# Kernel optimization log

Measured on AMD Instinct MI355X. Metric: run time of the kernel, lower is better.

## Reference

```python
import jax, jax.numpy as jnp
import numpy as np

N_NODES = 100000
N_EDGES = 1600000
D_IN = 128
D_HID = 128
D_OUT = 128
ORIG = 90000


def setup_inputs() -> dict:
    key = jax.random.key(0)
    ks = jax.random.split(key, 8)
    x = jax.random.normal(ks[0], (N_NODES, D_IN), dtype=jnp.float32)
    edge_index = jax.random.randint(ks[1], (2, N_EDGES), 0, N_NODES, dtype=jnp.int64)
    # Glorot-ish scaled weights; PyG SAGEConv: lin_l (with bias) on aggregated, lin_r (no bias) on root
    s1 = 1.0 / np.sqrt(D_IN)
    s2 = 1.0 / np.sqrt(D_HID)
    Wl1 = jax.random.normal(ks[2], (D_IN, D_HID), dtype=jnp.float32) * s1
    bl1 = jnp.zeros((D_HID,), dtype=jnp.float32)
    Wr1 = jax.random.normal(ks[3], (D_IN, D_HID), dtype=jnp.float32) * s1
    Wl2 = jax.random.normal(ks[4], (D_HID, D_OUT), dtype=jnp.float32) * s2
    bl2 = jnp.zeros((D_OUT,), dtype=jnp.float32)
    Wr2 = jax.random.normal(ks[5], (D_HID, D_OUT), dtype=jnp.float32) * s2
    return {"x": x, "edge_index": edge_index, "original_size": ORIG,
            "Wl1": Wl1, "bl1": bl1, "Wr1": Wr1,
            "Wl2": Wl2, "bl2": bl2, "Wr2": Wr2}


def _sage_conv(x, src, dst, Wl, bl, Wr):
    # PyG SAGEConv (aggr='mean'): out = lin_l(mean_{j in N(i)} x_j) + lin_r(x_i)
    n = x.shape[0]
    msgs = x[src]                                            # [E, d] gather
    ssum = jax.ops.segment_sum(msgs, dst, num_segments=n)    # [N, d]
    cnt = jax.ops.segment_sum(jnp.ones((src.shape[0],), dtype=x.dtype), dst,
                              num_segments=n)                # [N]
    mean = ssum / jnp.maximum(cnt, 1.0)[:, None]             # 0 for isolated nodes
    return mean @ Wl + bl + x @ Wr


def reference(x, edge_index, original_size, Wl1, bl1, Wr1, Wl2, bl2, Wr2):
    src, dst = edge_index[0], edge_index[1]
    h = _sage_conv(x, src, dst, Wl1, bl1, Wr1)
    h = _sage_conv(h, src, dst, Wl2, bl2, Wr2)
    return h[:original_size]
```

## Files before the change

### kernel.cpp

```cpp
#include <hip/hip_runtime.h>

#define NN 100000
#define DD 128

typedef __attribute__((ext_vector_type(8))) short bf16x8;
typedef __attribute__((ext_vector_type(4))) float f32x4;

__device__ __forceinline__ float bf2f(unsigned short u) {
    union { unsigned int i; float f; } v;
    v.i = ((unsigned int)u) << 16;
    return v.f;
}

__device__ __forceinline__ unsigned short f2bf(float f) {
    union { float f; unsigned int i; } v;
    v.f = f;
    unsigned int x = v.i;
    return (unsigned short)((x + 0x7FFFu + ((x >> 16) & 1u)) >> 16);
}

__device__ __forceinline__ float2 load2(const float* p, int i2) {
    return ((const float2*)p)[i2];
}

__device__ __forceinline__ bf16x8 load8_bf(const unsigned short* p) {
    return *((const bf16x8*)p);
}
__device__ __forceinline__ bf16x8 load8_bf(const float* p) {
    float4 a = ((const float4*)p)[0];
    float4 b = ((const float4*)p)[1];
    bf16x8 r;
    r[0] = (short)f2bf(a.x); r[1] = (short)f2bf(a.y);
    r[2] = (short)f2bf(a.z); r[3] = (short)f2bf(a.w);
    r[4] = (short)f2bf(b.x); r[5] = (short)f2bf(b.y);
    r[6] = (short)f2bf(b.z); r[7] = (short)f2bf(b.w);
    return r;
}


#define PCH 16
#define NBUKMAX 512
#define CAP 12288

__global__ __launch_bounds__(256) void hist_buckets(
    const int* __restrict__ ei, int E, int* __restrict__ bcnt, int nbuk) {
    __shared__ int is64_s;
    __shared__ int hl[NBUKMAX];
    int tid = threadIdx.x;
    for (int i = tid; i < nbuk; i += 256) hl[i] = 0;
    if (tid < 64) {
        int ok = (ei[2 * tid + 1] == 0);
        int all = __all(ok);
        if (tid == 0) is64_s = all;
    }
    __syncthreads();
    int is64 = is64_s;
    int e0 = blockIdx.x * (256 * PCH) + tid;
#pragma unroll
    for (int c = 0; c < PCH; c++) {
        int e = e0 + c * 256;
        if (e < E) {
            int d = is64 ? ei[2 * (E + e)] : ei[E + e];
            atomicAdd(&hl[d >> 8], 1);
        }
    }
    __syncthreads();
    for (int i = tid; i < nbuk; i += 256) {
        int v = hl[i];
        if (v) atomicAdd(&bcnt[i], v);
    }
}

__global__ void scan_buckets(const int* __restrict__ bcnt, int nbuk,
                             int* __restrict__ boff, int* __restrict__ offN, int E) {
    __shared__ int wsum[8];
    int tid = threadIdx.x;
    int lane = tid & 63, wid = tid >> 6;
    int v = (tid < nbuk) ? bcnt[tid] : 0;
    int s = v;
#pragma unroll
    for (int dl = 1; dl < 64; dl <<= 1) {
        int t = __shfl_up(s, dl, 64);
        if (lane >= dl) s += t;
    }
    if (lane == 63) wsum[wid] = s;
    __syncthreads();
    int w = 0;
#pragma unroll
    for (int i = 0; i < 8; i++) w += (i < wid) ? wsum[i] : 0;
    if (tid < nbuk) boff[tid] = w + s - v;
    if (tid == nbuk - 1) boff[nbuk] = w + s;
    if (tid == 0) offN[0] = E;
}

__global__ __launch_bounds__(256) void partition_edges(
    const int* __restrict__ ei, int E, const int* __restrict__ boff,
    int* __restrict__ bcur, unsigned long long* __restrict__ pairs, int nbuk) {
    __shared__ int is64_s;
    __shared__ int cntb[NBUKMAX];
    __shared__ int baseb[NBUKMAX];
    __shared__ int boffb[NBUKMAX];
    int tid = threadIdx.x;
    for (int i = tid; i < nbuk; i += 256) {
        cntb[i] = 0;
        boffb[i] = boff[i];
    }
    if (tid < 64) {
        int ok = (ei[2 * tid + 1] == 0);
        int all = __all(ok);
        if (tid == 0) is64_s = all;
    }
    __syncthreads();
    int is64 = is64_s;
    int e0 = blockIdx.x * (256 * PCH) + tid;

    int dv[PCH], sv[PCH], bl[PCH];
    bool va[PCH];
#pragma unroll
    for (int c = 0; c < PCH; c++) {
        int e = e0 + c * 256;
        va[c] = (e < E);
        dv[c] = va[c] ? (is64 ? ei[2 * (E + e)] : ei[E + e]) : 0;
        sv[c] = va[c] ? (is64 ? ei[2 * e] : ei[e]) : 0;
        bl[c] = 0;
    }
#pragma unroll
    for (int c = 0; c < PCH; c++) {
        if (va[c]) {
            int b = dv[c] >> 8;
            int l = atomicAdd(&cntb[b], 1);
            bl[c] = (b << 16) | l;
        }
    }
    __syncthreads();
    for (int i = tid; i < nbuk; i += 256) {
        int cb = cntb[i];
        baseb[i] = cb ? atomicAdd(&bcur[i], cb) : 0;
    }
    __syncthreads();
#pragma unroll
    for (int c = 0; c < PCH; c++) {
        if (va[c]) {
            int b = bl[c] >> 16, l = bl[c] & 0xffff;
            pairs[(size_t)(boffb[b] + baseb[b] + l)] =
                ((unsigned long long)(unsigned int)dv[c] << 32) | (unsigned int)sv[c];
        }
    }
}

__global__ __launch_bounds__(256) void build_csr(
    const unsigned long long* __restrict__ pairs, const int* __restrict__ boff,
    int* __restrict__ off, int* __restrict__ csr, int* __restrict__ cur, int N) {
    int b = blockIdx.x;
    int lo = b << 8;
    if (lo >= N) return;
    int hi = min(lo + 256, N);
    int nn = hi - lo;
    int base = boff[b];
    int pcount = boff[b + 1] - base;

    __shared__ int cnt_l[256];
    __shared__ int start_l[256];
    __shared__ int cur_l[256];
    __shared__ int wsum[4];
    __shared__ int lds_csr[CAP];

    int tid = threadIdx.x;
    cnt_l[tid] = 0;
    __syncthreads();

    for (int i = tid; i < pcount; i += 256) {
        int d = (int)(pairs[base + i] >> 32);
        atomicAdd(&cnt_l[d - lo], 1);
    }
    __syncthreads();

    int v = cnt_l[tid];
    int s = v;
    int lane = tid & 63, wid = tid >> 6;
#pragma unroll
    for (int dl = 1; dl < 64; dl <<= 1) {
        int t = __shfl_up(s, dl, 64);
        if (lane >= dl) s += t;
    }
    if (lane == 63) wsum[wid] = s;
    __syncthreads();
    int w = 0;
#pragma unroll
    for (int i = 0; i < 4; i++) w += (i < wid) ? wsum[i] : 0;
    int excl = w + s - v;
    start_l[tid] = excl;
    cur_l[tid] = excl;
    if (tid < nn) off[lo + tid] = base + excl;
    __syncthreads();

    if (pcount <= CAP) {
        for (int i = tid; i < pcount; i += 256) {
            unsigned long long p = pairs[base + i];
            int d = (int)(p >> 32) - lo;
            int pos = atomicAdd(&cur_l[d], 1);
            lds_csr[pos] = (int)(p & 0xffffffffu);
        }
        __syncthreads();
        for (int i = tid; i < pcount; i += 256) csr[base + i] = lds_csr[i];
    } else {
        for (int i = tid; i < pcount; i += 256) {
            unsigned long long p = pairs[base + i];
            int dg = (int)(p >> 32);
            int q = atomicAdd(&cur[dg], 1);
            csr[base + start_l[dg - lo] + q] = (int)(p & 0xffffffffu);
        }
    }
}

__global__ void cast_bf16(const float* __restrict__ in, unsigned short* __restrict__ out,
                          int n4) {
    int i = blockIdx.x * blockDim.x + threadIdx.x;
    if (i >= n4) return;
    float4 v = ((const float4*)in)[i];
    ushort4 o;
    o.x = f2bf(v.x); o.y = f2bf(v.y); o.z = f2bf(v.z); o.w = f2bf(v.w);
    ((ushort4*)out)[i] = o;
}

__global__ void prep_weights(const float* __restrict__ Wl1, const float* __restrict__ Wr1,
                             const float* __restrict__ Wl2, const float* __restrict__ Wr2,
                             unsigned short* __restrict__ Wt1, unsigned short* __restrict__ Wt2) {
    __shared__ float t[32][33];
    int which = blockIdx.x >> 4;
    const float* W = (which == 0) ? Wl1 : (which == 1) ? Wr1 : (which == 2) ? Wl2 : Wr2;
    unsigned short* Wt = (which < 2) ? Wt1 : Wt2;
    int koff = (which & 1) * 128;
    int b = blockIdx.x & 15;
    int bx = b & 3, by = b >> 2;
    int c = threadIdx.x & 31, r8 = threadIdx.x >> 5;
#pragma unroll
    for (int i = 0; i < 4; i++) {
        int r = r8 + i * 8;
        t[r][c] = W[(by * 32 + r) * 128 + bx * 32 + c];
    }
    __syncthreads();
#pragma unroll
    for (int i = 0; i < 4; i++) {
        int r = r8 + i * 8;
        Wt[(bx * 32 + r) * 256 + koff + by * 32 + c] = f2bf(t[c][r]);
    }
}

__global__ __launch_bounds__(256) void aggregate_bf(
    const unsigned short* __restrict__ feat,
    const int* __restrict__ off, const int* __restrict__ csr,
    unsigned short* __restrict__ mean, int N, const int* __restrict__ limp) {
    int lim = limp ? min(N, limp[0]) : N;
    int node = blockIdx.x * (blockDim.x >> 6) + (threadIdx.x >> 6);
    if (node >= lim) return;
    int lane = threadIdx.x & 63;
    int e = lane >> 4, q = lane & 15;
    int s0 = off[node], s1 = off[node + 1];

    float acc[8];
#pragma unroll
    for (int t = 0; t < 8; t++) acc[t] = 0.f;

    int j = s0 + e;
    while (j + 4 < s1) {
        int sa = csr[j];
        int sb = csr[j + 4];
        bf16x8 va = *((const bf16x8*)(feat + (size_t)sa * 128 + q * 8));
        bf16x8 vb = *((const bf16x8*)(feat + (size_t)sb * 128 + q * 8));
#pragma unroll
        for (int t = 0; t < 8; t++) acc[t] += bf2f((unsigned short)va[t]);
#pragma unroll
        for (int t = 0; t < 8; t++) acc[t] += bf2f((unsigned short)vb[t]);
        j += 8;
    }
    if (j < s1) {
        int sa = csr[j];
        bf16x8 va = *((const bf16x8*)(feat + (size_t)sa * 128 + q * 8));
#pragma unroll
        for (int t = 0; t < 8; t++) acc[t] += bf2f((unsigned short)va[t]);
    }

#pragma unroll
    for (int t = 0; t < 8; t++) {
        acc[t] += __shfl_xor(acc[t], 16, 64);
        acc[t] += __shfl_xor(acc[t], 32, 64);
    }

    int deg = s1 - s0;
    float inv = (deg > 0) ? (1.0f / (float)deg) : 0.0f;
    if (e == 0) {
        bf16x8 o;
#pragma unroll
        for (int t = 0; t < 8; t++) o[t] = (short)f2bf(acc[t] * inv);
        *((bf16x8*)(mean + (size_t)node * 128 + q * 8)) = o;
    }
}

__global__ void aggregate_f32(const float* __restrict__ feat,
                              const int* __restrict__ off, const int* __restrict__ csr,
                              unsigned short* __restrict__ mean, int N) {
    int node = blockIdx.x * (blockDim.x >> 6) + (threadIdx.x >> 6);
    if (node >= N) return;
    int lane = threadIdx.x & 63;
    int s0 = off[node], s1 = off[node + 1];
    float ax = 0.f, ay = 0.f;
    for (int j = s0; j < s1; j++) {
        int s = csr[j];
        float2 v = load2(feat, s * 64 + lane);
        ax += v.x; ay += v.y;
    }
    float inv = (s1 > s0) ? (1.0f / (float)(s1 - s0)) : 0.0f;
    unsigned int p = (unsigned int)f2bf(ax * inv) | ((unsigned int)f2bf(ay * inv) << 16);
    ((unsigned int*)mean)[node * 64 + lane] = p;
}

template <typename TA2, typename TO>
__global__ __launch_bounds__(256) void gemm_mfma(
    const unsigned short* __restrict__ A1, const TA2* __restrict__ A2,
    const unsigned short* __restrict__ Wt, const float* __restrict__ bias,
    TO* __restrict__ out, int Arows, int Nlimit, const int* __restrict__ origp) {
    int lim = Nlimit;
    if (origp) lim = min(lim, origp[0]);
    int n0 = blockIdx.x * 64;
    if (n0 >= lim) return;

    __shared__ unsigned short A_lds[64 * 40];

    int tid = threadIdx.x;
    int lane = tid & 63;
    int wid = tid >> 6;
    int wm = wid >> 1, wn = wid & 1;
    int qd = lane >> 4, l16 = lane & 15;

    f32x4 acc[2][4];
#pragma unroll
    for (int a = 0; a < 2; a++)
#pragma unroll
        for (int b = 0; b < 4; b++) acc[a][b] = (f32x4){0.f, 0.f, 0.f, 0.f};

    int srow = tid >> 2, sq = tid & 3;

    for (int ks = 0; ks < 8; ks++) {
        int phase = ks >> 2;
        int kb = (ks & 3) * 32;
        __syncthreads();
        {
            int gn = n0 + srow;
            bf16x8 v = (bf16x8){0, 0, 0, 0, 0, 0, 0, 0};
            if (gn < Arows) {
                if (phase)
                    v = load8_bf(A2 + gn * 128 + kb + sq * 8);
                else
                    v = load8_bf(A1 + gn * 128 + kb + sq * 8);
            }
            *((bf16x8*)(A_lds + srow * 40 + sq * 8)) = v;
        }
        __syncthreads();

        bf16x8 afrag[2];
#pragma unroll
        for (int tm = 0; tm < 2; tm++)
            afrag[tm] = *((const bf16x8*)(A_lds + (wm * 32 + tm * 16 + l16) * 40 + qd * 8));
#pragma unroll
        for (int tn = 0; tn < 4; tn++) {
            int f = wn * 64 + tn * 16 + l16;
            bf16x8 bfrag = *((const bf16x8*)(Wt + f * 256 + ks * 32 + qd * 8));
            acc[0][tn] = __builtin_amdgcn_mfma_f32_16x16x32_bf16(afrag[0], bfrag, acc[0][tn], 0, 0, 0);
            acc[1][tn] = __builtin_amdgcn_mfma_f32_16x16x32_bf16(afrag[1], bfrag, acc[1][tn], 0, 0, 0);
        }
    }

#pragma unroll
    for (int tn = 0; tn < 4; tn++) {
        int f = wn * 64 + tn * 16 + l16;
        float bv = bias[f];
#pragma unroll
        for (int tm = 0; tm < 2; tm++) {
#pragma unroll
            for (int r = 0; r < 4; r++) {
                int n = n0 + wm * 32 + tm * 16 + qd * 4 + r;
                if (n < lim) {
                    float val = acc[tm][tn][r] + bv;
                    if constexpr (__is_same(TO, float))
                        out[n * 128 + f] = val;
                    else
                        out[n * 128 + f] = f2bf(val);
                }
            }
        }
    }
}

extern "C" void kernel_launch(void* const* d_in, const int* in_sizes, int n_in,
                              void* d_out, int out_size, void* d_ws, size_t ws_size,
                              hipStream_t stream) {
    const float* x   = (const float*)d_in[0];
    const int*   ei  = (const int*)d_in[1];
    const int*   org = (const int*)d_in[2];
    const float* Wl1 = (const float*)d_in[3];
    const float* bl1 = (const float*)d_in[4];
    const float* Wr1 = (const float*)d_in[5];
    const float* Wl2 = (const float*)d_in[6];
    const float* bl2 = (const float*)d_in[7];
    const float* Wr2 = (const float*)d_in[8];
    float* out = (float*)d_out;

    const int N = in_sizes[0] / DD;
    const int E = in_sizes[1] / 2;

    size_t szFeat = (size_t)N * DD * 2;
    size_t szBase = 2 * szFeat
                  + 2 * 65536
                  + (size_t)N * 4 + 4096
                  + (size_t)(N + 1) * 4
                  + 4096
                  + (size_t)E * 4;
    bool big = ws_size >= szBase + szFeat + 4096;

    char* ws = (char*)d_ws;
    unsigned short* mean = (unsigned short*)ws;  ws += szFeat;
    unsigned short* h    = (unsigned short*)ws;  ws += szFeat;
    unsigned short* xb   = nullptr;
    if (big) { xb = (unsigned short*)ws; ws += szFeat; }
    unsigned short* Wt1 = (unsigned short*)ws;  ws += 65536;
    unsigned short* Wt2 = (unsigned short*)ws;  ws += 65536;
    int* cur  = (int*)ws;  ws += (size_t)N * 4;
    int* bcnt = (int*)ws;  ws += 2048;
    int* bcur = (int*)ws;  ws += 2048;
    int* off  = (int*)ws;  ws += (size_t)(N + 1) * 4;
    int* boff = (int*)ws;  ws += 4096;
    int* csr  = (int*)ws;

    unsigned long long* pairs = (unsigned long long*)mean;

    int nbuk = (N + 255) >> 8;
    int edgeGrid = (E + 256 * PCH - 1) / (256 * PCH);

    hipMemsetAsync(cur, 0, (size_t)N * 4 + 4096, stream);
    hist_buckets<<<edgeGrid, 256, 0, stream>>>(ei, E, bcnt, nbuk);
    scan_buckets<<<1, 512, 0, stream>>>(bcnt, nbuk, boff, off + N, E);
    partition_edges<<<edgeGrid, 256, 0, stream>>>(ei, E, boff, bcur, pairs, nbuk);
    build_csr<<<nbuk, 256, 0, stream>>>(pairs, boff, off, csr, cur, N);

    prep_weights<<<64, 256, 0, stream>>>(Wl1, Wr1, Wl2, Wr2, Wt1, Wt2);

    int aggGrid  = (N + 3) / 4;
    int gemmGrid = (N + 63) / 64;

    if (big) {
        cast_bf16<<<(N * DD / 4 + 255) / 256, 256, 0, stream>>>(x, xb, N * DD / 4);
        aggregate_bf<<<aggGrid, 256, 0, stream>>>(xb, off, csr, mean, N, nullptr);
        gemm_mfma<unsigned short, unsigned short><<<gemmGrid, 256, 0, stream>>>(
            mean, xb, Wt1, bl1, h, N, N, nullptr);
    } else {
        aggregate_f32<<<aggGrid, 256, 0, stream>>>(x, off, csr, mean, N);
        gemm_mfma<float, unsigned short><<<gemmGrid, 256, 0, stream>>>(
            mean, x, Wt1, bl1, h, N, N, nullptr);
    }
    aggregate_bf<<<aggGrid, 256, 0, stream>>>(h, off, csr, mean, N, org);
    gemm_mfma<unsigned short, float><<<gemmGrid, 256, 0, stream>>>(
        mean, h, Wt2, bl2, out, N, N, org);
}
```

Before: 371.2 us.

## Batch CSR index loads per wave and software-pipeline neighbor gathers in aggregation

The bf16 mean-aggregation kernel now loads up to 64 neighbor indices with one coalesced read per wave and hands them out with shuffles. It then gathers four neighbor rows per lane per step, prefetching the next batch before accumulating the current one. Accumulation uses packed float2 bf16-to-f32 conversion, and the cross-lane reduction shuffles doubles. The aim is more memory-level parallelism and fewer dependent index loads in the gather. The cost is more registers and extra shuffle work.

```diff
diff --git a/kernel.cpp b/kernel.cpp
--- a/kernel.cpp
+++ b/kernel.cpp
@@ -5,6 +5,7 @@
 
 typedef __attribute__((ext_vector_type(8))) short bf16x8;
 typedef __attribute__((ext_vector_type(4))) float f32x4;
+typedef __attribute__((ext_vector_type(2))) float f32x2;
 
 __device__ __forceinline__ float bf2f(unsigned short u) {
     union { unsigned int i; float f; } v;
@@ -21,6 +22,13 @@
 
 __device__ __forceinline__ float2 load2(const float* p, int i2) {
     return ((const float2*)p)[i2];
+}
+
+__device__ __forceinline__ f32x2 cvt2(unsigned int u) {
+    union { unsigned int i; float f; } lo, hi;
+    lo.i = u << 16;
+    hi.i = u & 0xffff0000u;
+    return (f32x2){lo.f, hi.f};
 }
 
 __device__ __forceinline__ bf16x8 load8_bf(const unsigned short* p) {
@@ -247,44 +255,62 @@
     }
 }
 
+#define ACC8(u) do { \
+    acc[0] += cvt2((u).x); acc[1] += cvt2((u).y); \
+    acc[2] += cvt2((u).z); acc[3] += cvt2((u).w); } while (0)
+
 __global__ __launch_bounds__(256) void aggregate_bf(
     const unsigned short* __restrict__ feat,
     const int* __restrict__ off, const int* __restrict__ csr,
     unsigned short* __restrict__ mean, int N, const int* __restrict__ limp) {
     int lim = limp ? min(N, limp[0]) : N;
-    int node = blockIdx.x * (blockDim.x >> 6) + (threadIdx.x >> 6);
+    int node = blockIdx.x * 4 + (threadIdx.x >> 6);
     if (node >= lim) return;
     int lane = threadIdx.x & 63;
     int e = lane >> 4, q = lane & 15;
     int s0 = off[node], s1 = off[node + 1];
 
-    float acc[8];
-#pragma unroll
-    for (int t = 0; t < 8; t++) acc[t] = 0.f;
-
-    int j = s0 + e;
-    while (j + 4 < s1) {
-        int sa = csr[j];
-        int sb = csr[j + 4];
-        bf16x8 va = *((const bf16x8*)(feat + (size_t)sa * 128 + q * 8));
-        bf16x8 vb = *((const bf16x8*)(feat + (size_t)sb * 128 + q * 8));
-#pragma unroll
-        for (int t = 0; t < 8; t++) acc[t] += bf2f((unsigned short)va[t]);
-#pragma unroll
-        for (int t = 0; t < 8; t++) acc[t] += bf2f((unsigned short)vb[t]);
-        j += 8;
-    }
-    if (j < s1) {
-        int sa = csr[j];
-        bf16x8 va = *((const bf16x8*)(feat + (size_t)sa * 128 + q * 8));
-#pragma unroll
-        for (int t = 0; t < 8; t++) acc[t] += bf2f((unsigned short)va[t]);
-    }
-
-#pragma unroll
-    for (int t = 0; t < 8; t++) {
-        acc[t] += __shfl_xor(acc[t], 16, 64);
-        acc[t] += __shfl_xor(acc[t], 32, 64);
+    f32x2 acc[4];
+#pragma unroll
+    for (int t = 0; t < 4; t++) acc[t] = (f32x2){0.f, 0.f};
+
+    for (int c0 = s0; c0 < s1; c0 += 64) {
+        int cdeg = min(64, s1 - c0);
+        int cr = (lane < cdeg) ? csr[c0 + lane] : 0;
+        int nb = (cdeg + 15) >> 4;
+
+        uint4 C0 = make_uint4(0, 0, 0, 0), C1 = C0, C2 = C0, C3 = C0;
+        {
+            int i0 = e, i1 = e + 4, i2 = e + 8, i3 = e + 12;
+            int t0 = __shfl(cr, i0, 64), t1 = __shfl(cr, i1, 64),
+                t2 = __shfl(cr, i2, 64), t3 = __shfl(cr, i3, 64);
+            if (i0 < cdeg) C0 = *((const uint4*)(feat + (size_t)t0 * 128 + q * 8));
+            if (i1 < cdeg) C1 = *((const uint4*)(feat + (size_t)t1 * 128 + q * 8));
+            if (i2 < cdeg) C2 = *((const uint4*)(feat + (size_t)t2 * 128 + q * 8));
+            if (i3 < cdeg) C3 = *((const uint4*)(feat + (size_t)t3 * 128 + q * 8));
+        }
+        for (int b = 1; b < nb; b++) {
+            int i0 = b * 16 + e, i1 = i0 + 4, i2 = i0 + 8, i3 = i0 + 12;
+            int t0 = __shfl(cr, i0, 64), t1 = __shfl(cr, i1, 64),
+                t2 = __shfl(cr, i2, 64), t3 = __shfl(cr, i3, 64);
+            uint4 N0 = make_uint4(0, 0, 0, 0), N1 = N0, N2 = N0, N3 = N0;
+            if (i0 < cdeg) N0 = *((const uint4*)(feat + (size_t)t0 * 128 + q * 8));
+            if (i1 < cdeg) N1 = *((const uint4*)(feat + (size_t)t1 * 128 + q * 8));
+            if (i2 < cdeg) N2 = *((const uint4*)(feat + (size_t)t2 * 128 + q * 8));
+            if (i3 < cdeg) N3 = *((const uint4*)(feat + (size_t)t3 * 128 + q * 8));
+            ACC8(C0); ACC8(C1); ACC8(C2); ACC8(C3);
+            C0 = N0; C1 = N1; C2 = N2; C3 = N3;
+        }
+        ACC8(C0); ACC8(C1); ACC8(C2); ACC8(C3);
+    }
+
+#pragma unroll
+    for (int t = 0; t < 4; t++) {
+        union { f32x2 v; double d; } a, b;
+        a.v = acc[t];
+        b.d = __shfl_xor(a.d, 16, 64); a.v += b.v;
+        b.d = __shfl_xor(a.d, 32, 64); a.v += b.v;
+        acc[t] = a.v;
     }
 
     int deg = s1 - s0;
@@ -292,7 +318,10 @@
     if (e == 0) {
         bf16x8 o;
 #pragma unroll
-        for (int t = 0; t < 8; t++) o[t] = (short)f2bf(acc[t] * inv);
+        for (int t = 0; t < 4; t++) {
+            o[2 * t]     = (short)f2bf(acc[t].x * inv);
+            o[2 * t + 1] = (short)f2bf(acc[t].y * inv);
+        }
         *((bf16x8*)(mean + (size_t)node * 128 + q * 8)) = o;
     }
 }
```

Result: no change. 364.8 us (-1.7%).
